# Performance work log

Measured on AMD Instinct MI355X. Metric: run time of the kernel, lower is better.

Reference implementation:

```python
import jax, jax.numpy as jnp
import numpy as np

TEMPERATURE = 1.0 / 0.07  # fixed (temperature_trainable=False)
B, D = 256, 65536


def setup_inputs() -> dict:
    key = jax.random.key(0)
    kA, kB = jax.random.split(key)
    feat_A = jax.random.normal(kA, (B, D), dtype=jnp.float32)
    feat_B = jax.random.normal(kB, (B, D), dtype=jnp.float32)
    # L2-normalize (standard for contrastive features; keeps exp(logits) finite)
    feat_A = feat_A / jnp.linalg.norm(feat_A, axis=-1, keepdims=True)
    feat_B = feat_B / jnp.linalg.norm(feat_B, axis=-1, keepdims=True)
    return {"feat_A": feat_A, "feat_B": feat_B}


def reference(feat_A, feat_B):
    # logits[i, j] = <A_i, B_j> * temperature   -- [B, B]
    logits = jnp.einsum("id,jd->ij", feat_A, feat_B) * TEMPERATURE
    pos_logits = jnp.diagonal(logits)  # [B]
    # margin=0.0, dcl=False, index=None -> neg_mask is all True, so
    # log(sum_j exp(logits)) is a full-row/col logsumexp (stable form of exp->sum->log)
    neg_A2B = jax.nn.logsumexp(logits, axis=1)  # A -> B classification
    neg_B2A = jax.nn.logsumexp(logits, axis=0)  # B -> A classification
    loss_A2B = jnp.mean(neg_A2B - pos_logits)
    loss_B2A = jnp.mean(neg_B2A - pos_logits)
    return (loss_A2B + loss_B2A) * 0.5
```

## Files before the change

kernel.cpp:

```cpp
#include <hip/hip_runtime.h>
#include <hip/hip_bf16.h>


#define D_DIM 65536
#define B_DIM 256
#define LDK 72

constexpr float TEMP = 1.0f / 0.07f;

typedef short short8 __attribute__((ext_vector_type(8)));
typedef float floatx4 __attribute__((ext_vector_type(4)));

__device__ inline unsigned short f2bf(float f) {
  unsigned u = __builtin_bit_cast(unsigned, f);
  unsigned rounding = 0x7fffu + ((u >> 16) & 1u);
  return (unsigned short)((u + rounding) >> 16);
}

__device__ inline void st_bf16x4(unsigned short* dst, float4 v) {
  uint2 u;
  u.x = (unsigned)f2bf(v.x) | ((unsigned)f2bf(v.y) << 16);
  u.y = (unsigned)f2bf(v.z) | ((unsigned)f2bf(v.w) << 16);
  *(uint2*)dst = u;
}

__global__ __launch_bounds__(256, 2) void gemm_splitk(
    const float* __restrict__ A, const float* __restrict__ Bm,
    float* __restrict__ partials, int Kc) {
  const int bid = blockIdx.x;
  const int mt = (bid & 1) * 128;
  const int nt = ((bid >> 1) & 1) * 128;
  const int chunk = bid >> 2;
  const size_t k0 = (size_t)chunk * (size_t)Kc;

  __shared__ unsigned short As[128][LDK];
  __shared__ unsigned short Bs[128][LDK];

  const int t = threadIdx.x;
  const int lane = t & 63;
  const int w = t >> 6;
  const int wm = (w & 1) * 64;
  const int wn = (w >> 1) * 64;

  const int lr = t >> 4;
  const int lc = (t & 15) * 4;

  const float* Abase = A + (size_t)(mt + lr) * D_DIM + k0 + lc;
  const float* Bbase = Bm + (size_t)(nt + lr) * D_DIM + k0 + lc;

  floatx4 acc[4][4];
#pragma unroll
  for (int mb = 0; mb < 4; ++mb)
#pragma unroll
    for (int nb = 0; nb < 4; ++nb) acc[mb][nb] = (floatx4)0.f;

  float4 ra[8], rb[8];
  const int nst = Kc >> 6;

#pragma unroll
  for (int p = 0; p < 8; ++p) {
    ra[p] = *(const float4*)(Abase + (size_t)p * 16 * D_DIM);
    rb[p] = *(const float4*)(Bbase + (size_t)p * 16 * D_DIM);
  }

  for (int s = 0; s < nst; ++s) {
#pragma unroll
    for (int p = 0; p < 8; ++p) {
      st_bf16x4(&As[lr + p * 16][lc], ra[p]);
      st_bf16x4(&Bs[lr + p * 16][lc], rb[p]);
    }
    __syncthreads();

    if (s + 1 < nst) {
      const float* Ap = Abase + (size_t)(s + 1) * 64;
      const float* Bp = Bbase + (size_t)(s + 1) * 64;
#pragma unroll
      for (int p = 0; p < 8; ++p) {
        ra[p] = *(const float4*)(Ap + (size_t)p * 16 * D_DIM);
        rb[p] = *(const float4*)(Bp + (size_t)p * 16 * D_DIM);
      }
    }

#pragma unroll
    for (int ks = 0; ks < 64; ks += 32) {
      short8 af[4], bf[4];
      const int ko = ks + (lane >> 4) * 8;
#pragma unroll
      for (int mb = 0; mb < 4; ++mb)
        af[mb] = *(const short8*)&As[wm + mb * 16 + (lane & 15)][ko];
#pragma unroll
      for (int nb = 0; nb < 4; ++nb)
        bf[nb] = *(const short8*)&Bs[wn + nb * 16 + (lane & 15)][ko];
#pragma unroll
      for (int mb = 0; mb < 4; ++mb)
#pragma unroll
        for (int nb = 0; nb < 4; ++nb)
          acc[mb][nb] = __builtin_amdgcn_mfma_f32_16x16x32_bf16(
              af[mb], bf[nb], acc[mb][nb], 0, 0, 0);
    }
    __syncthreads();
  }

  float* outp = partials + (size_t)chunk * (B_DIM * B_DIM);
#pragma unroll
  for (int mb = 0; mb < 4; ++mb) {
#pragma unroll
    for (int nb = 0; nb < 4; ++nb) {
      const int gi0 = mt + wm + mb * 16 + ((lane >> 4) * 4);
      const int gj = nt + wn + nb * 16 + (lane & 15);
#pragma unroll
      for (int r = 0; r < 4; ++r)
        outp[(size_t)(gi0 + r) * B_DIM + gj] = acc[mb][nb][r];
    }
  }
}

__global__ void reduce_rows(const float* __restrict__ partials,
                            float* __restrict__ logits,
                            float* __restrict__ out, int C) {
  const int i = blockIdx.x;
  const int j = threadIdx.x;
  const float* p = partials + (size_t)i * B_DIM + j;
  float s = 0.f;
#pragma unroll 4
  for (int c = 0; c < C; ++c) s += p[(size_t)c * (B_DIM * B_DIM)];
  const float lg = s * TEMP;
  logits[i * B_DIM + j] = lg;

  __shared__ float posv;
  if (j == i) posv = lg;

  float e = expf(lg);
#pragma unroll
  for (int off = 32; off > 0; off >>= 1) e += __shfl_down(e, off);
  __shared__ float wsum[4];
  if ((j & 63) == 0) wsum[j >> 6] = e;
  __syncthreads();
  if (j == 0) {
    const float tot = wsum[0] + wsum[1] + wsum[2] + wsum[3];
    atomicAdd(out, (logf(tot) - 2.f * posv) * (0.5f / 256.f));
  }
}

__global__ void reduce_cols(const float* __restrict__ logits,
                            float* __restrict__ out) {
  const int j = blockIdx.x;
  const int i = threadIdx.x;
  float e = expf(logits[(size_t)i * B_DIM + j]);
#pragma unroll
  for (int off = 32; off > 0; off >>= 1) e += __shfl_down(e, off);
  __shared__ float wsum[4];
  if ((i & 63) == 0) wsum[i >> 6] = e;
  __syncthreads();
  if (i == 0) {
    const float tot = wsum[0] + wsum[1] + wsum[2] + wsum[3];
    atomicAdd(out, logf(tot) * (0.5f / 256.f));
  }
}

extern "C" void kernel_launch(void* const* d_in, const int* in_sizes, int n_in,
                              void* d_out, int out_size, void* d_ws, size_t ws_size,
                              hipStream_t stream) {
  (void)in_sizes; (void)n_in; (void)out_size;
  const float* A = (const float*)d_in[0];
  const float* Bm = (const float*)d_in[1];
  float* out = (float*)d_out;

  const size_t per = (size_t)B_DIM * B_DIM * sizeof(float);
  int C = 128;
  while (C > 1 && (size_t)(C + 1) * per > ws_size) C >>= 1;
  const int Kc = D_DIM / C;

  float* logits = (float*)d_ws;
  float* partials = (float*)d_ws + (size_t)B_DIM * B_DIM;

  hipMemsetAsync(d_out, 0, sizeof(float), stream);
  gemm_splitk<<<4 * C, 256, 0, stream>>>(A, Bm, partials, Kc);
  reduce_rows<<<B_DIM, B_DIM, 0, stream>>>(partials, logits, out, C);
  reduce_cols<<<B_DIM, B_DIM, 0, stream>>>(logits, out);
}
```

Baseline: 172.1 us.

## Use 64x64 tiles with double-buffered LDS and parallelize split-K reduction

```diff
diff --git a/kernel.cpp b/kernel.cpp
--- a/kernel.cpp
+++ b/kernel.cpp
@@ -24,23 +24,25 @@
   *(uint2*)dst = u;
 }
 
-__global__ __launch_bounds__(256, 2) void gemm_splitk(
+__global__ __launch_bounds__(256, 4) void gemm_splitk(
     const float* __restrict__ A, const float* __restrict__ Bm,
-    float* __restrict__ partials, int Kc) {
+    float* __restrict__ partials, int Kc, int cshift) {
   const int bid = blockIdx.x;
-  const int mt = (bid & 1) * 128;
-  const int nt = ((bid >> 1) & 1) * 128;
-  const int chunk = bid >> 2;
+  const int chunk = bid & ((1 << cshift) - 1);
+  const int tile = bid >> cshift;
+  const int mt = (tile & 3) * 64;
+  const int nt = (tile >> 2) * 64;
   const size_t k0 = (size_t)chunk * (size_t)Kc;
 
-  __shared__ unsigned short As[128][LDK];
-  __shared__ unsigned short Bs[128][LDK];
+  __shared__ unsigned short As[2][64][LDK];
+  __shared__ unsigned short Bs[2][64][LDK];
 
   const int t = threadIdx.x;
   const int lane = t & 63;
   const int w = t >> 6;
-  const int wm = (w & 1) * 64;
-  const int wn = (w >> 1) * 64;
+  const int wm = w * 16;
+  const int lane15 = lane & 15;
+  const int laneq = lane >> 4;
 
   const int lr = t >> 4;
   const int lc = (t & 15) * 4;
@@ -48,26 +50,25 @@
   const float* Abase = A + (size_t)(mt + lr) * D_DIM + k0 + lc;
   const float* Bbase = Bm + (size_t)(nt + lr) * D_DIM + k0 + lc;
 
-  floatx4 acc[4][4];
+  floatx4 acc[4];
 #pragma unroll
-  for (int mb = 0; mb < 4; ++mb)
-#pragma unroll
-    for (int nb = 0; nb < 4; ++nb) acc[mb][nb] = (floatx4)0.f;
+  for (int nb = 0; nb < 4; ++nb) acc[nb] = (floatx4)0.f;
 
-  float4 ra[8], rb[8];
+  float4 ra[4], rb[4];
   const int nst = Kc >> 6;
 
 #pragma unroll
-  for (int p = 0; p < 8; ++p) {
+  for (int p = 0; p < 4; ++p) {
     ra[p] = *(const float4*)(Abase + (size_t)p * 16 * D_DIM);
     rb[p] = *(const float4*)(Bbase + (size_t)p * 16 * D_DIM);
   }
 
   for (int s = 0; s < nst; ++s) {
+    const int buf = s & 1;
 #pragma unroll
-    for (int p = 0; p < 8; ++p) {
-      st_bf16x4(&As[lr + p * 16][lc], ra[p]);
-      st_bf16x4(&Bs[lr + p * 16][lc], rb[p]);
+    for (int p = 0; p < 4; ++p) {
+      st_bf16x4(&As[buf][lr + p * 16][lc], ra[p]);
+      st_bf16x4(&Bs[buf][lr + p * 16][lc], rb[p]);
     }
     __syncthreads();
 
@@ -75,7 +76,7 @@
       const float* Ap = Abase + (size_t)(s + 1) * 64;
       const float* Bp = Bbase + (size_t)(s + 1) * 64;
 #pragma unroll
-      for (int p = 0; p < 8; ++p) {
+      for (int p = 0; p < 4; ++p) {
         ra[p] = *(const float4*)(Ap + (size_t)p * 16 * D_DIM);
         rb[p] = *(const float4*)(Bp + (size_t)p * 16 * D_DIM);
       }
@@ -83,35 +84,26 @@
 
 #pragma unroll
     for (int ks = 0; ks < 64; ks += 32) {
-      short8 af[4], bf[4];
-      const int ko = ks + (lane >> 4) * 8;
-#pragma unroll
-      for (int mb = 0; mb < 4; ++mb)
-        af[mb] = *(const short8*)&As[wm + mb * 16 + (lane & 15)][ko];
+      const int ko = ks + laneq * 8;
+      short8 af = *(const short8*)&As[buf][wm + lane15][ko];
+      short8 bf[4];
 #pragma unroll
       for (int nb = 0; nb < 4; ++nb)
-        bf[nb] = *(const short8*)&Bs[wn + nb * 16 + (lane & 15)][ko];
+        bf[nb] = *(const short8*)&Bs[buf][nb * 16 + lane15][ko];
 #pragma unroll
-      for (int mb = 0; mb < 4; ++mb)
-#pragma unroll
-        for (int nb = 0; nb < 4; ++nb)
-          acc[mb][nb] = __builtin_amdgcn_mfma_f32_16x16x32_bf16(
-              af[mb], bf[nb], acc[mb][nb], 0, 0, 0);
+      for (int nb = 0; nb < 4; ++nb)
+        acc[nb] = __builtin_amdgcn_mfma_f32_16x16x32_bf16(af, bf[nb], acc[nb], 0, 0, 0);
     }
-    __syncthreads();
   }
 
   float* outp = partials + (size_t)chunk * (B_DIM * B_DIM);
+  const int gi0 = mt + wm + laneq * 4;
 #pragma unroll
-  for (int mb = 0; mb < 4; ++mb) {
+  for (int nb = 0; nb < 4; ++nb) {
+    const int gj = nt + nb * 16 + lane15;
 #pragma unroll
-    for (int nb = 0; nb < 4; ++nb) {
-      const int gi0 = mt + wm + mb * 16 + ((lane >> 4) * 4);
-      const int gj = nt + wn + nb * 16 + (lane & 15);
-#pragma unroll
-      for (int r = 0; r < 4; ++r)
-        outp[(size_t)(gi0 + r) * B_DIM + gj] = acc[mb][nb][r];
-    }
+    for (int r = 0; r < 4; ++r)
+      outp[(size_t)(gi0 + r) * B_DIM + gj] = acc[nb][r];
   }
 }
 
@@ -119,12 +111,25 @@
                             float* __restrict__ logits,
                             float* __restrict__ out, int C) {
   const int i = blockIdx.x;
-  const int j = threadIdx.x;
-  const float* p = partials + (size_t)i * B_DIM + j;
-  float s = 0.f;
-#pragma unroll 4
-  for (int c = 0; c < C; ++c) s += p[(size_t)c * (B_DIM * B_DIM)];
-  const float lg = s * TEMP;
+  const int t = threadIdx.x;
+  const int slice = t >> 6;
+  const int col4 = (t & 63) * 4;
+
+  const int cper = C >> 2;
+  const float* p = partials + (size_t)(slice * cper) * (B_DIM * B_DIM) +
+                   (size_t)i * B_DIM + col4;
+  float4 s = make_float4(0.f, 0.f, 0.f, 0.f);
+#pragma unroll 8
+  for (int c = 0; c < cper; ++c) {
+    float4 v = *(const float4*)(p + (size_t)c * (B_DIM * B_DIM));
+    s.x += v.x; s.y += v.y; s.z += v.z; s.w += v.w;
+  }
+  __shared__ float sbuf[4][B_DIM];
+  *(float4*)&sbuf[slice][col4] = s;
+  __syncthreads();
+
+  const int j = t;
+  const float lg = (sbuf[0][j] + sbuf[1][j] + sbuf[2][j] + sbuf[3][j]) * TEMP;
   logits[i * B_DIM + j] = lg;
 
   __shared__ float posv;
@@ -167,15 +172,17 @@
   float* out = (float*)d_out;
 
   const size_t per = (size_t)B_DIM * B_DIM * sizeof(float);
-  int C = 128;
-  while (C > 1 && (size_t)(C + 1) * per > ws_size) C >>= 1;
+  int C = 64;
+  while (C > 4 && (size_t)(C + 1) * per > ws_size) C >>= 1;
   const int Kc = D_DIM / C;
+  int cshift = 0;
+  while ((1 << cshift) < C) ++cshift;
 
   float* logits = (float*)d_ws;
   float* partials = (float*)d_ws + (size_t)B_DIM * B_DIM;
 
   hipMemsetAsync(d_out, 0, sizeof(float), stream);
-  gemm_splitk<<<4 * C, 256, 0, stream>>>(A, Bm, partials, Kc);
+  gemm_splitk<<<16 * C, 256, 0, stream>>>(A, Bm, partials, Kc, cshift);
   reduce_rows<<<B_DIM, B_DIM, 0, stream>>>(partials, logits, out, C);
   reduce_cols<<<B_DIM, B_DIM, 0, stream>>>(logits, out);
 }
```

After: 181.6 us. +5.6%, slower.
